# Performance work log

Hardware: AMD Instinct MI355X
Metric: run time of the kernel (lower is better)

## Reference

```python
import jax, jax.numpy as jnp
import numpy as np

N = 200000   # total nodes
E = 800000   # total edges
G = 4096     # number of graphs
DIM_DRUG = 78
GNN = 128


def batch_norm(x, g, b, m, v):
    # eval-mode BatchNorm1d
    return (x - m) * jax.lax.rsqrt(v + 1e-5) * g + b


def gin_conv(x, edge_index, w1, b1, w2, b2):
    # PyG GINConv, eps=0: out = MLP((1+eps)*x + sum_{j->i} x_j)
    agg = jax.ops.segment_sum(x[edge_index[0]], edge_index[1], num_segments=N)
    h = x + agg
    return jax.nn.relu(h @ w1 + b1) @ w2 + b2


def gcn_conv(x, edge_index, w, b):
    # PyG GCNConv with added self-loops and symmetric normalization
    xw = x @ w  # [N, out]
    loop = jnp.arange(N, dtype=edge_index.dtype)
    src = jnp.concatenate([edge_index[0], loop])
    dst = jnp.concatenate([edge_index[1], loop])
    deg = jax.ops.segment_sum(jnp.ones_like(dst, dtype=xw.dtype), dst, num_segments=N)
    dinv = jnp.where(deg > 0, deg ** -0.5, 0.0)
    msg = xw[src] * (dinv[src] * dinv[dst])[:, None]
    return jax.ops.segment_sum(msg, dst, num_segments=N) + b


def segment_softmax(scores, seg):
    m = jax.ops.segment_max(scores, seg, num_segments=G)
    e = jnp.exp(scores - m[seg])
    z = jax.ops.segment_sum(e, seg, num_segments=G)
    return e / z[seg]


def sag_pool(x, edge_index, batch, gcn_w, gcn_b):
    scores = jnp.tanh(gcn_conv(x, edge_index, gcn_w, gcn_b)[:, 0])
    norm = segment_softmax(scores, batch)
    pooled = jax.ops.segment_sum(x * norm[:, None], batch, num_segments=G)
    return pooled


def setup_inputs() -> dict:
    key = jax.random.key(0)
    ks = jax.random.split(key, 24)
    d = {}
    d['drug_feature'] = jax.random.normal(ks[0], (N, DIM_DRUG), jnp.float32)
    d['edge_index'] = jax.random.randint(ks[1], (2, E), 0, N, jnp.int64 if jax.config.jax_enable_x64 else jnp.int32)
    d['ibatch'] = jnp.sort(jax.random.randint(ks[2], (N,), 0, G, jnp.int32))
    # BatchNorm params (eval mode)
    d['bn0_g'] = jax.random.uniform(ks[3], (DIM_DRUG,), jnp.float32, 0.5, 1.5)
    d['bn0_b'] = jax.random.normal(ks[4], (DIM_DRUG,)) * 0.1
    d['bn0_m'] = jax.random.normal(ks[5], (DIM_DRUG,)) * 0.1
    d['bn0_v'] = jax.random.uniform(ks[6], (DIM_DRUG,), jnp.float32, 0.5, 1.5)
    d['bn1_g'] = jax.random.uniform(ks[7], (GNN,), jnp.float32, 0.5, 1.5)
    d['bn1_b'] = jax.random.normal(ks[8], (GNN,)) * 0.1
    d['bn1_m'] = jax.random.normal(ks[9], (GNN,)) * 0.1
    d['bn1_v'] = jax.random.uniform(ks[10], (GNN,), jnp.float32, 0.5, 1.5)
    d['bn2_g'] = jax.random.uniform(ks[11], (GNN,), jnp.float32, 0.5, 1.5)
    d['bn2_b'] = jax.random.normal(ks[12], (GNN,)) * 0.1
    d['bn2_m'] = jax.random.normal(ks[13], (GNN,)) * 0.1
    d['bn2_v'] = jax.random.uniform(ks[14], (GNN,), jnp.float32, 0.5, 1.5)
    # GIN MLPs
    s1 = (2.0 / DIM_DRUG) ** 0.5
    d['gin1_w1'] = jax.random.normal(ks[15], (DIM_DRUG, 2 * GNN)) * s1
    d['gin1_b1'] = jnp.zeros((2 * GNN,), jnp.float32)
    d['gin1_w2'] = jax.random.normal(ks[16], (2 * GNN, GNN)) * (2.0 / (2 * GNN)) ** 0.5
    d['gin1_b2'] = jnp.zeros((GNN,), jnp.float32)
    d['gin2_w1'] = jax.random.normal(ks[17], (GNN, 2 * GNN)) * (2.0 / GNN) ** 0.5
    d['gin2_b1'] = jnp.zeros((2 * GNN,), jnp.float32)
    d['gin2_w2'] = jax.random.normal(ks[18], (2 * GNN, GNN)) * (2.0 / (2 * GNN)) ** 0.5
    d['gin2_b2'] = jnp.zeros((GNN,), jnp.float32)
    # SAG pooling GCN scorers (out_channels=1)
    d['gcn1_w'] = jax.random.normal(ks[19], (GNN, 1)) * (1.0 / GNN) ** 0.5
    d['gcn1_b'] = jnp.zeros((1,), jnp.float32)
    d['gcn2_w'] = jax.random.normal(ks[20], (GNN, 1)) * (1.0 / GNN) ** 0.5
    d['gcn2_b'] = jnp.zeros((1,), jnp.float32)
    return d


def reference(drug_feature, bn0_g, bn0_b, bn0_m, bn0_v,
              gin1_w1, gin1_b1, gin1_w2, gin1_b2, bn1_g, bn1_b, bn1_m, bn1_v,
              gin2_w1, gin2_b1, gin2_w2, gin2_b2, bn2_g, bn2_b, bn2_m, bn2_v,
              gcn1_w, gcn1_b, gcn2_w, gcn2_b, edge_index, ibatch):
    x = batch_norm(drug_feature, bn0_g, bn0_b, bn0_m, bn0_v)
    h1 = gin_conv(x, edge_index, gin1_w1, gin1_b1, gin1_w2, gin1_b2)
    h1 = batch_norm(jax.nn.relu(h1), bn1_g, bn1_b, bn1_m, bn1_v)  # dropout = identity (eval)
    h2 = gin_conv(h1, edge_index, gin2_w1, gin2_b1, gin2_w2, gin2_b2)
    h2 = batch_norm(jax.nn.relu(h2), bn2_g, bn2_b, bn2_m, bn2_v)
    g1 = sag_pool(h1, edge_index, ibatch, gcn1_w, gcn1_b)
    g2 = sag_pool(h2, edge_index, ibatch, gcn2_w, gcn2_b)
    return jnp.stack((g1, g2), axis=1)  # [G, 2, GNN]
```

## Files before the change

kernel.cpp:

```cpp
#include <hip/hip_runtime.h>
#include <hip/hip_bf16.h>

typedef __hip_bfloat16 bf16;
typedef __attribute__((ext_vector_type(8))) short short8;
typedef __attribute__((ext_vector_type(4))) float f32x4;

#define NN 200000
#define EE 800000
#define GG 4096
#define DD 78
#define HH 128
#define CAP 24
#define ZR NN

__device__ __forceinline__ float b2f(bf16 x) { return __bfloat162float(x); }
__device__ __forceinline__ bf16 f2b(float x) { return __float2bfloat16(x); }
__device__ __forceinline__ unsigned short f2u(float f) {
    bf16 h = __float2bfloat16(f);
    return __builtin_bit_cast(unsigned short, h);
}
__device__ __forceinline__ float u2f(unsigned int u) {
    return __builtin_bit_cast(float, u << 16);
}

constexpr size_t OFF_CNT   = 0;
constexpr size_t OFF_ELL   = OFF_CNT  + (size_t)NN * 4;
constexpr size_t OFF_H1    = OFF_ELL  + (size_t)NN * CAP * 4;
constexpr size_t OFF_H2    = OFF_H1   + (size_t)(NN + 64) * HH * 2;
constexpr size_t OFF_X96   = OFF_H2;
constexpr size_t OFF_DINV  = OFF_H2   + (size_t)NN * HH * 2;
constexpr size_t OFF_SP1   = OFF_DINV + (size_t)NN * 4;
constexpr size_t OFF_SP2   = OFF_SP1  + (size_t)NN * 4;
constexpr size_t OFF_E1    = OFF_SP2  + (size_t)NN * 4;
constexpr size_t OFF_E2    = OFF_E1   + (size_t)NN * 4;
constexpr size_t OFF_START = OFF_E2   + (size_t)NN * 4;
constexpr size_t OFF_P1A   = OFF_START + 16640;
constexpr size_t OFF_P1B   = OFF_P1A  + 24576 * 2;
constexpr size_t OFF_P2A   = OFF_P1B  + 32768 * 2;
constexpr size_t OFF_P2B   = OFF_P2A  + 32768 * 2;
constexpr size_t OFF_END   = OFF_P2B  + 32768 * 2;


__global__ void ell_build(const int* __restrict__ src, const int* __restrict__ dst,
                          int* __restrict__ cnt, int* __restrict__ ell) {
    int e = blockIdx.x * 256 + threadIdx.x;
    if (e >= EE) return;
    int t = dst[e];
    int slot = atomicAdd(&cnt[t], 1);
    if (slot < CAP) ell[t * CAP + slot] = src[e];
}

__global__ void dinv_kernel(const int* __restrict__ cnt, float* __restrict__ dinv,
                            bf16* __restrict__ H1) {
    int i = blockIdx.x * 256 + threadIdx.x;
    if (i < NN) dinv[i] = rsqrtf((float)cnt[i] + 1.0f);
    if (i < HH) H1[(size_t)ZR * HH + i] = f2b(0.f);
}

__global__ void start_kernel(const int* __restrict__ ibatch, int* __restrict__ startg) {
    int i = blockIdx.x * 256 + threadIdx.x;
    if (i >= NN) return;
    int b = ibatch[i];
    int pb = (i == 0) ? -1 : ibatch[i - 1];
    for (int g = pb + 1; g <= b; g++) startg[g] = i;
    if (i == NN - 1) {
        for (int g = b + 1; g <= GG; g++) startg[g] = NN;
    }
}

__global__ void x96_prep(const float* __restrict__ feat, const float* __restrict__ g,
                         const float* __restrict__ b, const float* __restrict__ m,
                         const float* __restrict__ v, bf16* __restrict__ X96) {
    int idx = blockIdx.x * 256 + threadIdx.x;
    if (idx >= (NN + 1) * 96) return;
    int row = idx / 96, col = idx - row * 96;
    float out = 0.f;
    if (row < NN && col < DD) {
        float s = g[col] * rsqrtf(v[col] + 1e-5f);
        out = feat[(size_t)row * DD + col] * s + (b[col] - m[col] * s);
    }
    X96[idx] = f2b(out);
}

__global__ void pack_w(const float* __restrict__ w, bf16* __restrict__ wp,
                       int Krows, int Ncols, int total) {
    int idx = blockIdx.x * 256 + threadIdx.x;
    if (idx >= total) return;
    int j = idx & 7;
    int l = (idx >> 3) & 63;
    int f = idx >> 9;
    int CT = Ncols >> 4;
    int ct = f % CT;
    int ks = f / CT;
    int k = ks * 32 + (l >> 4) * 8 + j;
    int n = ct * 16 + (l & 15);
    float val = (k < Krows) ? w[(size_t)k * Ncols + n] : 0.0f;
    wp[idx] = f2b(val);
}

template <int K, int KS1>
__launch_bounds__(256, 4)
__global__ void gin_mfma(const bf16* __restrict__ xin,
                         const int* __restrict__ ell, const int* __restrict__ cnt,
                         const bf16* __restrict__ pA, const float* __restrict__ b1,
                         const bf16* __restrict__ pB, const float* __restrict__ b2,
                         const float* __restrict__ bng, const float* __restrict__ bnb,
                         const float* __restrict__ bnm, const float* __restrict__ bnv,
                         const float* __restrict__ gcnw,
                         bf16* __restrict__ hout, float* __restrict__ SP) {
    __shared__ short hld[32][K + 8];
    __shared__ short hid[32][264];
    const int tid  = threadIdx.x;
    const int lane = tid & 63;
    const int w    = tid >> 6;
    const int l15  = lane & 15;
    const int q4   = lane >> 4;
    const int row0 = blockIdx.x * 32;

    if (K == 128 || l15 < 12) {
        const int qd = l15 * 8;
        const short* base = (const short*)xin;
#pragma unroll
        for (int t = 0; t < 2; t++) {
            const int lr = w * 8 + t * 4 + q4;
            const int node = row0 + lr;
            int c = cnt[node]; if (c > CAP) c = CAP;
            uint4 u = *(const uint4*)(base + (size_t)node * K + qd);
            float a0 = u2f(u.x), a1 = u2f(u.x >> 16);
            float a2 = u2f(u.y), a3 = u2f(u.y >> 16);
            float a4 = u2f(u.z), a5 = u2f(u.z >> 16);
            float a6 = u2f(u.w), a7 = u2f(u.w >> 16);
            for (int kk = 0; kk < c; kk += 4) {
                int4 ss = *(const int4*)(ell + node * CAP + kk);
                int s0 = ss.x;
                int s1 = (kk + 1 < c) ? ss.y : ZR;
                int s2 = (kk + 2 < c) ? ss.z : ZR;
                int s3 = (kk + 3 < c) ? ss.w : ZR;
                uint4 u0 = *(const uint4*)(base + (size_t)s0 * K + qd);
                uint4 u1 = *(const uint4*)(base + (size_t)s1 * K + qd);
                uint4 u2 = *(const uint4*)(base + (size_t)s2 * K + qd);
                uint4 u3 = *(const uint4*)(base + (size_t)s3 * K + qd);
                a0 += u2f(u0.x) + u2f(u1.x) + u2f(u2.x) + u2f(u3.x);
                a1 += u2f(u0.x >> 16) + u2f(u1.x >> 16) + u2f(u2.x >> 16) + u2f(u3.x >> 16);
                a2 += u2f(u0.y) + u2f(u1.y) + u2f(u2.y) + u2f(u3.y);
                a3 += u2f(u0.y >> 16) + u2f(u1.y >> 16) + u2f(u2.y >> 16) + u2f(u3.y >> 16);
                a4 += u2f(u0.z) + u2f(u1.z) + u2f(u2.z) + u2f(u3.z);
                a5 += u2f(u0.z >> 16) + u2f(u1.z >> 16) + u2f(u2.z >> 16) + u2f(u3.z >> 16);
                a6 += u2f(u0.w) + u2f(u1.w) + u2f(u2.w) + u2f(u3.w);
                a7 += u2f(u0.w >> 16) + u2f(u1.w >> 16) + u2f(u2.w >> 16) + u2f(u3.w >> 16);
            }
            uint4 o;
            o.x = (unsigned)f2u(a0) | ((unsigned)f2u(a1) << 16);
            o.y = (unsigned)f2u(a2) | ((unsigned)f2u(a3) << 16);
            o.z = (unsigned)f2u(a4) | ((unsigned)f2u(a5) << 16);
            o.w = (unsigned)f2u(a6) | ((unsigned)f2u(a7) << 16);
            *(uint4*)&hld[lr][qd] = o;
        }
    }
    __syncthreads();

    {
        f32x4 acc[2][4];
#pragma unroll
        for (int ct = 0; ct < 4; ct++) {
            float bv = b1[w * 64 + ct * 16 + l15];
            acc[0][ct] = (f32x4){bv, bv, bv, bv};
            acc[1][ct] = (f32x4){bv, bv, bv, bv};
        }
#pragma unroll
        for (int ks = 0; ks < KS1; ks++) {
            short8 fa0 = *(const short8*)&hld[l15][ks * 32 + q4 * 8];
            short8 fa1 = *(const short8*)&hld[16 + l15][ks * 32 + q4 * 8];
#pragma unroll
            for (int ct = 0; ct < 4; ct++) {
                int cg = w * 4 + ct;
                short8 fb = *(const short8*)((const short*)pA + (((size_t)(ks * 16 + cg) * 64 + lane) << 3));
                acc[0][ct] = __builtin_amdgcn_mfma_f32_16x16x32_bf16(fa0, fb, acc[0][ct], 0, 0, 0);
                acc[1][ct] = __builtin_amdgcn_mfma_f32_16x16x32_bf16(fa1, fb, acc[1][ct], 0, 0, 0);
            }
        }
#pragma unroll
        for (int rt = 0; rt < 2; rt++)
#pragma unroll
            for (int ct = 0; ct < 4; ct++)
#pragma unroll
                for (int r = 0; r < 4; r++) {
                    int row = rt * 16 + q4 * 4 + r;
                    int col = w * 64 + ct * 16 + l15;
                    hid[row][col] = (short)f2u(fmaxf(acc[rt][ct][r], 0.0f));
                }
    }
    __syncthreads();

    {
        f32x4 acc2[2][2];
#pragma unroll
        for (int ct = 0; ct < 2; ct++) {
            float bv = b2[w * 32 + ct * 16 + l15];
            acc2[0][ct] = (f32x4){bv, bv, bv, bv};
            acc2[1][ct] = (f32x4){bv, bv, bv, bv};
        }
#pragma unroll
        for (int ks = 0; ks < 8; ks++) {
            short8 fa0 = *(const short8*)&hid[l15][ks * 32 + q4 * 8];
            short8 fa1 = *(const short8*)&hid[16 + l15][ks * 32 + q4 * 8];
#pragma unroll
            for (int ct = 0; ct < 2; ct++) {
                int cg = w * 2 + ct;
                short8 fb = *(const short8*)((const short*)pB + (((size_t)(ks * 8 + cg) * 64 + lane) << 3));
                acc2[0][ct] = __builtin_amdgcn_mfma_f32_16x16x32_bf16(fa0, fb, acc2[0][ct], 0, 0, 0);
                acc2[1][ct] = __builtin_amdgcn_mfma_f32_16x16x32_bf16(fa1, fb, acc2[1][ct], 0, 0, 0);
            }
        }
        float p[2][4] = {{0.f, 0.f, 0.f, 0.f}, {0.f, 0.f, 0.f, 0.f}};
#pragma unroll
        for (int ct = 0; ct < 2; ct++) {
            int col = w * 32 + ct * 16 + l15;
            float s  = bng[col] * rsqrtf(bnv[col] + 1e-5f);
            float sh = bnb[col] - bnm[col] * s;
            float gw = gcnw[col];
#pragma unroll
            for (int rt = 0; rt < 2; rt++)
#pragma unroll
                for (int r = 0; r < 4; r++) {
                    float vv = fmaxf(acc2[rt][ct][r], 0.0f) * s + sh;
                    int row = rt * 16 + q4 * 4 + r;
                    hout[(size_t)(row0 + row) * HH + col] = f2b(vv);
                    p[rt][r] += vv * gw;
                }
        }
#pragma unroll
        for (int rt = 0; rt < 2; rt++)
#pragma unroll
            for (int r = 0; r < 4; r++) {
                float v = p[rt][r];
                v += __shfl_xor(v, 1);
                v += __shfl_xor(v, 2);
                v += __shfl_xor(v, 4);
                v += __shfl_xor(v, 8);
                if (l15 == 0) atomicAdd(&SP[row0 + rt * 16 + q4 * 4 + r], v);
            }
    }
}


__global__ void finalize_kernel(const float* __restrict__ sp1, const float* __restrict__ sp2,
                                const float* __restrict__ dinv,
                                const int* __restrict__ ell, const int* __restrict__ cnt,
                                const float* __restrict__ gb1, const float* __restrict__ gb2,
                                float* __restrict__ e1, float* __restrict__ e2) {
    int i = blockIdx.x * 256 + threadIdx.x;
    if (i >= NN) return;
    float di = dinv[i];
    int c = cnt[i];
    if (c > CAP) c = CAP;
    float a1 = sp1[i] * di, a2 = sp2[i] * di;
    for (int k = 0; k < c; k++) {
        int s = ell[i * CAP + k];
        float f = dinv[s];
        a1 += sp1[s] * f;
        a2 += sp2[s] * f;
    }
    float sc1 = tanhf(a1 * di + gb1[0]);
    float sc2 = tanhf(a2 * di + gb2[0]);
    e1[i] = expf(sc1);
    e2[i] = expf(sc2);
}

__global__ void pool_kernel(const bf16* __restrict__ H1, const bf16* __restrict__ H2,
                            const float* __restrict__ e1, const float* __restrict__ e2,
                            const int* __restrict__ startg, float* __restrict__ out) {
    int g = blockIdx.x;
    int lo = startg[g], hi = startg[g + 1];
    int tid = threadIdx.x;

    float z1 = 0.f, z2 = 0.f;
    for (int i = lo + tid; i < hi; i += 128) { z1 += e1[i]; z2 += e2[i]; }
    __shared__ float red[256];
    red[tid] = z1; red[128 + tid] = z2;
    __syncthreads();
    if (tid == 0) {
        float a = 0.f, b = 0.f;
        for (int t = 0; t < 128; t++) { a += red[t]; b += red[128 + t]; }
        red[0] = a; red[128] = b;
    }
    __syncthreads();
    float inv1 = red[0]   > 0.f ? 1.0f / red[0]   : 0.f;
    float inv2 = red[128] > 0.f ? 1.0f / red[128] : 0.f;

    float acc1 = 0.f, acc2 = 0.f;
    for (int i = lo; i < hi; i++) {
        float w1 = e1[i], w2 = e2[i];
        acc1 += b2f(H1[(size_t)i * HH + tid]) * w1;
        acc2 += b2f(H2[(size_t)i * HH + tid]) * w2;
    }
    out[(size_t)(g * 2 + 0) * HH + tid] = acc1 * inv1;
    out[(size_t)(g * 2 + 1) * HH + tid] = acc2 * inv2;
}

__global__ void zero_out_kernel(float* __restrict__ out, int n) {
    int i = blockIdx.x * 256 + threadIdx.x;
    if (i < n) out[i] = 0.f;
}

extern "C" void kernel_launch(void* const* d_in, const int* in_sizes, int n_in,
                              void* d_out, int out_size, void* d_ws, size_t ws_size,
                              hipStream_t stream) {
    const float* feat   = (const float*)d_in[0];
    const int*   ei     = (const int*)d_in[1];
    const int*   ibatch = (const int*)d_in[2];
    const float* bn0_g = (const float*)d_in[3],  *bn0_b = (const float*)d_in[4];
    const float* bn0_m = (const float*)d_in[5],  *bn0_v = (const float*)d_in[6];
    const float* bn1_g = (const float*)d_in[7],  *bn1_b = (const float*)d_in[8];
    const float* bn1_m = (const float*)d_in[9],  *bn1_v = (const float*)d_in[10];
    const float* bn2_g = (const float*)d_in[11], *bn2_b = (const float*)d_in[12];
    const float* bn2_m = (const float*)d_in[13], *bn2_v = (const float*)d_in[14];
    const float* g1w1 = (const float*)d_in[15], *g1b1 = (const float*)d_in[16];
    const float* g1w2 = (const float*)d_in[17], *g1b2 = (const float*)d_in[18];
    const float* g2w1 = (const float*)d_in[19], *g2b1 = (const float*)d_in[20];
    const float* g2w2 = (const float*)d_in[21], *g2b2 = (const float*)d_in[22];
    const float* gcn1_w = (const float*)d_in[23], *gcn1_b = (const float*)d_in[24];
    const float* gcn2_w = (const float*)d_in[25], *gcn2_b = (const float*)d_in[26];

    float* outp = (float*)d_out;

    if (ws_size < OFF_END) {
        zero_out_kernel<<<(out_size + 255) / 256, 256, 0, stream>>>(outp, out_size);
        return;
    }

    char* ws = (char*)d_ws;
    int*   CNT    = (int*)(ws + OFF_CNT);
    int*   ELL    = (int*)(ws + OFF_ELL);
    bf16*  H1     = (bf16*)(ws + OFF_H1);
    bf16*  H2     = (bf16*)(ws + OFF_H2);
    bf16*  X96    = (bf16*)(ws + OFF_X96);
    float* DINV   = (float*)(ws + OFF_DINV);
    float* SP1    = (float*)(ws + OFF_SP1);
    float* SP2    = (float*)(ws + OFF_SP2);
    float* E1     = (float*)(ws + OFF_E1);
    float* E2     = (float*)(ws + OFF_E2);
    int*   STARTG = (int*)(ws + OFF_START);
    bf16*  P1A    = (bf16*)(ws + OFF_P1A);
    bf16*  P1B    = (bf16*)(ws + OFF_P1B);
    bf16*  P2A    = (bf16*)(ws + OFF_P2A);
    bf16*  P2B    = (bf16*)(ws + OFF_P2B);

    const int* esrc = ei;
    const int* edst = ei + EE;

    hipMemsetAsync(CNT, 0, (size_t)NN * 4, stream);
    hipMemsetAsync(SP1, 0, (size_t)2 * NN * 4, stream);

    ell_build<<<(EE + 255) / 256, 256, 0, stream>>>(esrc, edst, CNT, ELL);
    dinv_kernel<<<(NN + 255) / 256, 256, 0, stream>>>(CNT, DINV, H1);
    start_kernel<<<(NN + 255) / 256, 256, 0, stream>>>(ibatch, STARTG);

    pack_w<<<(24576 + 255) / 256, 256, 0, stream>>>(g1w1, P1A, DD,  256, 24576);
    pack_w<<<(32768 + 255) / 256, 256, 0, stream>>>(g1w2, P1B, 256, 128, 32768);
    pack_w<<<(32768 + 255) / 256, 256, 0, stream>>>(g2w1, P2A, 128, 256, 32768);
    pack_w<<<(32768 + 255) / 256, 256, 0, stream>>>(g2w2, P2B, 256, 128, 32768);

    x96_prep<<<((NN + 1) * 96 + 255) / 256, 256, 0, stream>>>(feat, bn0_g, bn0_b, bn0_m, bn0_v, X96);

    gin_mfma<96, 3><<<NN / 32, 256, 0, stream>>>(X96, ELL, CNT, P1A, g1b1, P1B, g1b2,
                                                 bn1_g, bn1_b, bn1_m, bn1_v, gcn1_w, H1, SP1);
    gin_mfma<128, 4><<<NN / 32, 256, 0, stream>>>(H1, ELL, CNT, P2A, g2b1, P2B, g2b2,
                                                  bn2_g, bn2_b, bn2_m, bn2_v, gcn2_w, H2, SP2);

    finalize_kernel<<<(NN + 255) / 256, 256, 0, stream>>>(SP1, SP2, DINV, ELL, CNT,
                                                          gcn1_b, gcn2_b, E1, E2);
    pool_kernel<<<GG, 128, 0, stream>>>(H1, H2, E1, E2, STARTG, outp);
}
```

Measured before the change: 303.7 us.

## Fuse preprocessing kernels and memsets into one prep launch, recompute dinv inline

Merges the weight packing, counter/score zeroing, graph start computation, and BN0 feature prep into a single block-partitioned prep kernel, replacing two memsets and six launches. The feature prep now writes four bf16 values per thread with a vector store. The dinv array and its kernel are removed; finalize recomputes rsqrt of the degree from cnt for each node and neighbour. This cuts launch overhead and one pass over the nodes, at the cost of extra rsqrt work and cnt gathers in finalize.

```diff
diff --git a/kernel.cpp b/kernel.cpp
--- a/kernel.cpp
+++ b/kernel.cpp
@@ -4,6 +4,7 @@
 typedef __hip_bfloat16 bf16;
 typedef __attribute__((ext_vector_type(8))) short short8;
 typedef __attribute__((ext_vector_type(4))) float f32x4;
+typedef __attribute__((ext_vector_type(4))) unsigned short u16x4;
 
 #define NN 200000
 #define EE 800000
@@ -28,8 +29,7 @@
 constexpr size_t OFF_H1    = OFF_ELL  + (size_t)NN * CAP * 4;
 constexpr size_t OFF_H2    = OFF_H1   + (size_t)(NN + 64) * HH * 2;
 constexpr size_t OFF_X96   = OFF_H2;
-constexpr size_t OFF_DINV  = OFF_H2   + (size_t)NN * HH * 2;
-constexpr size_t OFF_SP1   = OFF_DINV + (size_t)NN * 4;
+constexpr size_t OFF_SP1   = OFF_H2   + (size_t)NN * HH * 2;
 constexpr size_t OFF_SP2   = OFF_SP1  + (size_t)NN * 4;
 constexpr size_t OFF_E1    = OFF_SP2  + (size_t)NN * 4;
 constexpr size_t OFF_E2    = OFF_E1   + (size_t)NN * 4;
@@ -41,51 +41,8 @@
 constexpr size_t OFF_END   = OFF_P2B  + 32768 * 2;
 
 
-__global__ void ell_build(const int* __restrict__ src, const int* __restrict__ dst,
-                          int* __restrict__ cnt, int* __restrict__ ell) {
-    int e = blockIdx.x * 256 + threadIdx.x;
-    if (e >= EE) return;
-    int t = dst[e];
-    int slot = atomicAdd(&cnt[t], 1);
-    if (slot < CAP) ell[t * CAP + slot] = src[e];
-}
-
-__global__ void dinv_kernel(const int* __restrict__ cnt, float* __restrict__ dinv,
-                            bf16* __restrict__ H1) {
-    int i = blockIdx.x * 256 + threadIdx.x;
-    if (i < NN) dinv[i] = rsqrtf((float)cnt[i] + 1.0f);
-    if (i < HH) H1[(size_t)ZR * HH + i] = f2b(0.f);
-}
-
-__global__ void start_kernel(const int* __restrict__ ibatch, int* __restrict__ startg) {
-    int i = blockIdx.x * 256 + threadIdx.x;
-    if (i >= NN) return;
-    int b = ibatch[i];
-    int pb = (i == 0) ? -1 : ibatch[i - 1];
-    for (int g = pb + 1; g <= b; g++) startg[g] = i;
-    if (i == NN - 1) {
-        for (int g = b + 1; g <= GG; g++) startg[g] = NN;
-    }
-}
-
-__global__ void x96_prep(const float* __restrict__ feat, const float* __restrict__ g,
-                         const float* __restrict__ b, const float* __restrict__ m,
-                         const float* __restrict__ v, bf16* __restrict__ X96) {
-    int idx = blockIdx.x * 256 + threadIdx.x;
-    if (idx >= (NN + 1) * 96) return;
-    int row = idx / 96, col = idx - row * 96;
-    float out = 0.f;
-    if (row < NN && col < DD) {
-        float s = g[col] * rsqrtf(v[col] + 1e-5f);
-        out = feat[(size_t)row * DD + col] * s + (b[col] - m[col] * s);
-    }
-    X96[idx] = f2b(out);
-}
-
-__global__ void pack_w(const float* __restrict__ w, bf16* __restrict__ wp,
-                       int Krows, int Ncols, int total) {
-    int idx = blockIdx.x * 256 + threadIdx.x;
-    if (idx >= total) return;
+__device__ __forceinline__ void pack_one(const float* __restrict__ w, bf16* __restrict__ wp,
+                                         int Krows, int Ncols, int idx) {
     int j = idx & 7;
     int l = (idx >> 3) & 63;
     int f = idx >> 9;
@@ -96,6 +53,69 @@
     int n = ct * 16 + (l & 15);
     float val = (k < Krows) ? w[(size_t)k * Ncols + n] : 0.0f;
     wp[idx] = f2b(val);
+}
+
+__global__ void prep(const float* __restrict__ feat,
+                     const float* __restrict__ g0, const float* __restrict__ b0,
+                     const float* __restrict__ m0, const float* __restrict__ v0,
+                     const float* __restrict__ w1a, const float* __restrict__ w1b,
+                     const float* __restrict__ w2a, const float* __restrict__ w2b,
+                     const int* __restrict__ ibatch,
+                     int* __restrict__ cnt, float* __restrict__ sp1, float* __restrict__ sp2,
+                     bf16* __restrict__ X96, bf16* __restrict__ H1,
+                     int* __restrict__ startg,
+                     bf16* __restrict__ P1A, bf16* __restrict__ P1B,
+                     bf16* __restrict__ P2A, bf16* __restrict__ P2B) {
+    const int b = blockIdx.x, tid = threadIdx.x;
+    if (b < 96) {
+        pack_one(w1a, P1A, DD, 256, b * 256 + tid);
+    } else if (b < 224) {
+        pack_one(w1b, P1B, 256, 128, (b - 96) * 256 + tid);
+    } else if (b < 352) {
+        pack_one(w2a, P2A, 128, 256, (b - 224) * 256 + tid);
+    } else if (b < 480) {
+        pack_one(w2b, P2B, 256, 128, (b - 352) * 256 + tid);
+    } else if (b < 1262) {
+        int i = (b - 480) * 256 + tid;
+        if (i < NN) { cnt[i] = 0; sp1[i] = 0.f; sp2[i] = 0.f; }
+    } else if (b < 1263) {
+        if (tid < HH) ((unsigned short*)H1)[(size_t)ZR * HH + tid] = 0;
+        if (tid < 96) ((unsigned short*)X96)[(size_t)ZR * 96 + tid] = 0;
+    } else if (b < 2045) {
+        int i = (b - 1263) * 256 + tid;
+        if (i < NN) {
+            int bb = ibatch[i];
+            int pb = (i == 0) ? -1 : ibatch[i - 1];
+            for (int g = pb + 1; g <= bb; g++) startg[g] = i;
+            if (i == NN - 1) {
+                for (int g = bb + 1; g <= GG; g++) startg[g] = NN;
+            }
+        }
+    } else {
+        int gi = (b - 2045) * 256 + tid;
+        int row = gi / 24;
+        int c0 = (gi - row * 24) * 4;
+        float o[4];
+#pragma unroll
+        for (int j = 0; j < 4; j++) {
+            int c = c0 + j;
+            if (c < DD) {
+                float s = g0[c] * rsqrtf(v0[c] + 1e-5f);
+                o[j] = feat[(size_t)row * DD + c] * s + (b0[c] - m0[c] * s);
+            } else o[j] = 0.f;
+        }
+        u16x4 st = {f2u(o[0]), f2u(o[1]), f2u(o[2]), f2u(o[3])};
+        *(u16x4*)((unsigned short*)X96 + (size_t)row * 96 + c0) = st;
+    }
+}
+
+__global__ void ell_build(const int* __restrict__ src, const int* __restrict__ dst,
+                          int* __restrict__ cnt, int* __restrict__ ell) {
+    int e = blockIdx.x * 256 + threadIdx.x;
+    if (e >= EE) return;
+    int t = dst[e];
+    int slot = atomicAdd(&cnt[t], 1);
+    if (slot < CAP) ell[t * CAP + slot] = src[e];
 }
 
 template <int K, int KS1>
@@ -243,21 +263,19 @@
     }
 }
 
-
 __global__ void finalize_kernel(const float* __restrict__ sp1, const float* __restrict__ sp2,
-                                const float* __restrict__ dinv,
                                 const int* __restrict__ ell, const int* __restrict__ cnt,
                                 const float* __restrict__ gb1, const float* __restrict__ gb2,
                                 float* __restrict__ e1, float* __restrict__ e2) {
     int i = blockIdx.x * 256 + threadIdx.x;
     if (i >= NN) return;
-    float di = dinv[i];
-    int c = cnt[i];
-    if (c > CAP) c = CAP;
+    int ci = cnt[i];
+    float di = rsqrtf((float)ci + 1.0f);
+    int c = ci > CAP ? CAP : ci;
     float a1 = sp1[i] * di, a2 = sp2[i] * di;
     for (int k = 0; k < c; k++) {
         int s = ell[i * CAP + k];
-        float f = dinv[s];
+        float f = rsqrtf((float)cnt[s] + 1.0f);
         a1 += sp1[s] * f;
         a2 += sp2[s] * f;
     }
@@ -335,7 +353,6 @@
     bf16*  H1     = (bf16*)(ws + OFF_H1);
     bf16*  H2     = (bf16*)(ws + OFF_H2);
     bf16*  X96    = (bf16*)(ws + OFF_X96);
-    float* DINV   = (float*)(ws + OFF_DINV);
     float* SP1    = (float*)(ws + OFF_SP1);
     float* SP2    = (float*)(ws + OFF_SP2);
     float* E1     = (float*)(ws + OFF_E1);
@@ -349,26 +366,18 @@
     const int* esrc = ei;
     const int* edst = ei + EE;
 
-    hipMemsetAsync(CNT, 0, (size_t)NN * 4, stream);
-    hipMemsetAsync(SP1, 0, (size_t)2 * NN * 4, stream);
-
+    prep<<<20795, 256, 0, stream>>>(feat, bn0_g, bn0_b, bn0_m, bn0_v,
+                                    g1w1, g1w2, g2w1, g2w2, ibatch,
+                                    CNT, SP1, SP2, X96, H1, STARTG,
+                                    P1A, P1B, P2A, P2B);
     ell_build<<<(EE + 255) / 256, 256, 0, stream>>>(esrc, edst, CNT, ELL);
-    dinv_kernel<<<(NN + 255) / 256, 256, 0, stream>>>(CNT, DINV, H1);
-    start_kernel<<<(NN + 255) / 256, 256, 0, stream>>>(ibatch, STARTG);
-
-    pack_w<<<(24576 + 255) / 256, 256, 0, stream>>>(g1w1, P1A, DD,  256, 24576);
-    pack_w<<<(32768 + 255) / 256, 256, 0, stream>>>(g1w2, P1B, 256, 128, 32768);
-    pack_w<<<(32768 + 255) / 256, 256, 0, stream>>>(g2w1, P2A, 128, 256, 32768);
-    pack_w<<<(32768 + 255) / 256, 256, 0, stream>>>(g2w2, P2B, 256, 128, 32768);
-
-    x96_prep<<<((NN + 1) * 96 + 255) / 256, 256, 0, stream>>>(feat, bn0_g, bn0_b, bn0_m, bn0_v, X96);
 
     gin_mfma<96, 3><<<NN / 32, 256, 0, stream>>>(X96, ELL, CNT, P1A, g1b1, P1B, g1b2,
                                                  bn1_g, bn1_b, bn1_m, bn1_v, gcn1_w, H1, SP1);
     gin_mfma<128, 4><<<NN / 32, 256, 0, stream>>>(H1, ELL, CNT, P2A, g2b1, P2B, g2b2,
                                                   bn2_g, bn2_b, bn2_m, bn2_v, gcn2_w, H2, SP2);
 
-    finalize_kernel<<<(NN + 255) / 256, 256, 0, stream>>>(SP1, SP2, DINV, ELL, CNT,
+    finalize_kernel<<<(NN + 255) / 256, 256, 0, stream>>>(SP1, SP2, ELL, CNT,
                                                           gcn1_b, gcn2_b, E1, E2);
     pool_kernel<<<GG, 128, 0, stream>>>(H1, H2, E1, E2, STARTG, outp);
 }
```

New measurement: 330.7 us. 1.09x slower.
